# Performance work log

Hardware: AMD Instinct MI355X
Metric: run time of the kernel (lower is better)

Reference implementation:

```python
import jax, jax.numpy as jnp
import numpy as np

V, T, K, L, D = 256, 256, 36, 32, 1024
TAU = 0.05
MODE = 0
NEG_INF = -jnp.inf


def setup_inputs() -> dict:
    key = jax.random.key(0)
    k1, k2 = jax.random.split(key)
    imgs = jax.random.normal(k1, (V, K, D), dtype=jnp.float32)
    caps = jax.random.normal(k2, (T, L, D), dtype=jnp.float32)
    # Full lengths: the original module writes -inf into sim and 0 into w at
    # padded positions, so padding would produce -inf*0 = NaN in the output.
    img_lens = jnp.full((V,), K, dtype=jnp.int32)
    cap_lens = jnp.full((T,), L, dtype=jnp.int32)
    return {"imgs": imgs, "caps": caps, "img_lens": img_lens, "cap_lens": cap_lens}


def _l2norm(x):
    return x / jnp.maximum(jnp.linalg.norm(x, axis=-1, keepdims=True), 1e-12)


def reference(imgs, caps, img_lens, cap_lens):
    # masks: [V,K], [T,L]
    img_mask = (jnp.arange(K)[None, :] < img_lens[:, None]).astype(imgs.dtype)
    cap_mask = (jnp.arange(L)[None, :] < cap_lens[:, None]).astype(caps.dtype)
    # AvePool: masked mean over valid tokens, then L2-normalize
    img_glo = _l2norm((imgs * img_mask[:, :, None]).sum(1) / img_lens[:, None].astype(imgs.dtype))
    cap_glo = _l2norm((caps * cap_mask[:, :, None]).sum(1) / cap_lens[:, None].astype(caps.dtype))
    # ds: [V,T,K], et: [V,T,L]  (computed as in the original; note the original
    # forward overwrites w with the masked sim, so ds/et/softmax do not affect
    # the returned value — we keep only the live dataflow here)
    ds = jnp.einsum('vkd,td->vtk', imgs, cap_glo)
    et = jnp.einsum('tld,vd->vtl', caps, img_glo)
    del ds, et  # dead in the original (w is reassigned to masked sim)
    # sim: [V,T,K,L]
    sim = jnp.einsum('vkd,tld->vtkl', imgs, caps)
    sim_mask = img_mask[:, None, :, None] * cap_mask[None, :, None, :]  # [V,T,K,L]
    valid = sim_mask != 0
    sim = jnp.where(valid, sim, NEG_INF)
    # final w in the original is sim.masked_fill(sim_mask == 0, 0)
    w = jnp.where(valid, sim, 0.0)
    return jnp.einsum('vtkl,vtkl->vt', sim, w)
```

## Files before the change

kernel.cpp:

```cpp
#include <hip/hip_runtime.h>

#define V_N 256
#define T_N 256
#define K_N 36
#define L_N 32
#define D_N 1024
#define MROWS (V_N * K_N)
#define NROWS (T_N * L_N)
#define BM 128
#define BN 128
#define BK 64
#define KSTEPS (D_N / BK)
#define NBM (MROWS / BM)
#define NBN (NROWS / BN)
#define NWG (NBM * NBN)

typedef __attribute__((ext_vector_type(8))) short bf16x8;
typedef __attribute__((ext_vector_type(4))) float f32x4;
typedef __attribute__((ext_vector_type(16))) float f32x16;

#define SB0 __builtin_amdgcn_sched_barrier(0)
#define BAR __builtin_amdgcn_s_barrier()

__device__ __forceinline__ ushort f2bf(float x) {
  union { float f; unsigned int u; } c; c.f = x;
  unsigned int r = c.u + 0x7FFFu + ((c.u >> 16) & 1u);
  return (ushort)(r >> 16);
}

__global__ void cvt_a(const float* __restrict__ imgs, ushort* __restrict__ aws) {
  const int AQ = MROWS * (D_N / 4);
  for (int q = blockIdx.x * blockDim.x + threadIdx.x; q < AQ;
       q += gridDim.x * blockDim.x) {
    float4 f = reinterpret_cast<const float4*>(imgs)[q];
    ushort4 u; u.x = f2bf(f.x); u.y = f2bf(f.y); u.z = f2bf(f.z); u.w = f2bf(f.w);
    reinterpret_cast<ushort4*>(aws)[q] = u;
  }
}

__global__ void cvt_b2(const float* __restrict__ caps, ushort* __restrict__ b2) {
  const int NH = 256 * 64;
  int gid = blockIdx.x * blockDim.x + threadIdx.x;
  int h = gid >> 6;
  int lane = gid & 63;
  if (h >= NH) return;
  int c = h >> 6;
  int s = h & 63;
  int col = c * 32 + (lane & 31);
  int k   = s * 16 + ((lane >> 5) << 3);
  const float4* src = reinterpret_cast<const float4*>(caps + (size_t)col * D_N + k);
  float4 f0 = src[0], f1 = src[1];
  union { ushort u[8]; int4 v4; } pk;
  pk.u[0] = f2bf(f0.x); pk.u[1] = f2bf(f0.y); pk.u[2] = f2bf(f0.z); pk.u[3] = f2bf(f0.w);
  pk.u[4] = f2bf(f1.x); pk.u[5] = f2bf(f1.y); pk.u[6] = f2bf(f1.z); pk.u[7] = f2bf(f1.w);
  *reinterpret_cast<int4*>(b2 + (size_t)h * 512 + lane * 8) = pk.v4;
}

__global__ __launch_bounds__(256, 3) void gemm3(
    const ushort* __restrict__ aws, const ushort* __restrict__ b2,
    float* __restrict__ out) {
  __shared__ ushort lds[2 * BM * BK];

  int orig = (int)blockIdx.x;
  int xcd = orig & 7;
  int idx = orig >> 3;
  const int bn = xcd * 8 + (idx & 7);
  const int bm = idx >> 3;
  const int row0 = bm * BM;
  const int col0 = bn * BN;

  const int tid  = (int)threadIdx.x;
  const int lane = tid & 63;
  const int wid  = tid >> 6;
  const int wr   = wid >> 1;
  const int wc   = wid & 1;

  auto stageA = [&](int kt) {
    ushort* buf = lds + (kt & 1) * (BM * BK);
#pragma unroll
    for (int it = 0; it < 4; ++it) {
      int q = it * 256 + tid;
      int r = q >> 3;
      int sw = ((q & 7) << 4) ^ ((r & 7) << 4);
      const ushort* ga = aws + (size_t)(row0 + r) * D_N + kt * BK + (sw >> 1);
      __builtin_amdgcn_global_load_lds(
          (const __attribute__((address_space(1))) void*)ga,
          (__attribute__((address_space(3))) void*)(buf + q * 8), 16, 0, 0);
    }
  };

  auto rdA = [&](const ushort* buf, int mt, int ks) -> bf16x8 {
    int r = wr * 64 + mt * 32 + (lane & 31);
    int cb = ks * 32 + ((lane >> 5) << 4);
    int sw = cb ^ ((r & 7) << 4);
    return *reinterpret_cast<const bf16x8*>(buf + r * 64 + (sw >> 1));
  };

  const ushort* bbase = b2 + ((size_t)(bn * 4 + wc * 2) * 64) * 512 + lane * 8;
  auto ldB = [&](int t, int nt, int ks) -> bf16x8 {
    return *reinterpret_cast<const bf16x8*>(
        bbase + ((size_t)nt * 64 + t * 4 + ks) * 512);
  };

  f32x16 acc[2][2];
#pragma unroll
  for (int mt = 0; mt < 2; ++mt)
#pragma unroll
    for (int nt = 0; nt < 2; ++nt)
#pragma unroll
      for (int j = 0; j < 16; ++j) acc[mt][nt][j] = 0.f;

  stageA(0);
  asm volatile("s_waitcnt vmcnt(0)" ::: "memory");
  SB0; BAR; SB0;

  for (int t = 0; t < KSTEPS; ++t) {
    const ushort* buf = lds + (t & 1) * (BM * BK);
    if (t < KSTEPS - 1) stageA(t + 1);

    bf16x8 bB[8], aA[8];
#pragma unroll
    for (int ks = 0; ks < 4; ++ks) {
      bB[ks * 2]     = ldB(t, 0, ks);
      bB[ks * 2 + 1] = ldB(t, 1, ks);
    }
#pragma unroll
    for (int ks = 0; ks < 4; ++ks) {
      aA[ks * 2]     = rdA(buf, 0, ks);
      aA[ks * 2 + 1] = rdA(buf, 1, ks);
    }

#pragma unroll
    for (int ks = 0; ks < 4; ++ks)
#pragma unroll
      for (int mt = 0; mt < 2; ++mt)
#pragma unroll
        for (int nt = 0; nt < 2; ++nt)
          acc[mt][nt] = __builtin_amdgcn_mfma_f32_32x32x16_bf16(
              aA[ks * 2 + mt], bB[ks * 2 + nt], acc[mt][nt], 0, 0, 0);

    asm volatile("s_waitcnt vmcnt(0)" ::: "memory");
    SB0; BAR; SB0;
  }

#pragma unroll
  for (int mt = 0; mt < 2; ++mt) {
    int gbase = row0 + wr * 64 + mt * 32;
    int v0 = gbase / K_N;
    int b = (v0 + 1) * K_N;
#pragma unroll
    for (int nt = 0; nt < 2; ++nt) {
      f32x16 a = acc[mt][nt];
      float s0 = 0.f, s1 = 0.f;
#pragma unroll
      for (int j = 0; j < 16; ++j) {
        int row = (j & 3) + 8 * (j >> 2) + 4 * (lane >> 5);
        float x = a[j];
        float x2 = x * x;
        if (gbase + row < b) s0 += x2; else s1 += x2;
      }
#pragma unroll
      for (int off = 32; off > 0; off >>= 1) {
        s0 += __shfl_xor(s0, off, 64);
        s1 += __shfl_xor(s1, off, 64);
      }
      if (lane == 0) {
        int tcol = (col0 + wc * 64 + nt * 32) >> 5;
        atomicAdd(out + v0 * T_N + tcol, s0);
        if (b < gbase + 32) atomicAdd(out + (v0 + 1) * T_N + tcol, s1);
      }
    }
  }
}

__global__ __launch_bounds__(256) void gemm_fb(
    const float* __restrict__ imgs, const float* __restrict__ caps,
    float* __restrict__ out) {
  __shared__ ushort lds[128 * 64 + 128 * 64];
  ushort* ldsA = lds;
  ushort* ldsB = lds + 128 * 64;
  const int NBMf = MROWS / 128, NBNf = NROWS / 128;
  int orig = (int)blockIdx.x;
  int xcd = orig & 7;
  int idx = orig >> 3;
  int bn = xcd * (NBNf / 8) + (idx % (NBNf / 8));
  int bm = idx / (NBNf / 8);
  const int row0 = bm * 128, col0 = bn * 128;
  const int tid = (int)threadIdx.x, lane = tid & 63, wid = tid >> 6;
  const int wr = wid >> 1, wc = wid & 1;
  f32x4 acc[4][4];
#pragma unroll
  for (int i = 0; i < 4; ++i)
#pragma unroll
    for (int j = 0; j < 4; ++j) acc[i][j] = (f32x4){0.f, 0.f, 0.f, 0.f};
  for (int kt = 0; kt < KSTEPS; ++kt) {
#pragma unroll
    for (int it = 0; it < 4; ++it) {
      int q = it * 256 + tid;
      int r = q >> 3;
      int sw = ((q & 7) << 4) ^ ((r & 7) << 4);
      const float4* src = reinterpret_cast<const float4*>(
          imgs + (size_t)(row0 + r) * D_N + kt * BK + (sw >> 1));
      float4 f0 = src[0], f1 = src[1];
      union { ushort u[8]; int4 v4; } pk;
      pk.u[0] = f2bf(f0.x); pk.u[1] = f2bf(f0.y); pk.u[2] = f2bf(f0.z); pk.u[3] = f2bf(f0.w);
      pk.u[4] = f2bf(f1.x); pk.u[5] = f2bf(f1.y); pk.u[6] = f2bf(f1.z); pk.u[7] = f2bf(f1.w);
      *reinterpret_cast<int4*>(ldsA + q * 8) = pk.v4;
    }
#pragma unroll
    for (int it = 0; it < 4; ++it) {
      int q = it * 256 + tid;
      int r = q >> 3;
      int sw = ((q & 7) << 4) ^ ((r & 7) << 4);
      const float4* src = reinterpret_cast<const float4*>(
          caps + (size_t)(col0 + r) * D_N + kt * BK + (sw >> 1));
      float4 f0 = src[0], f1 = src[1];
      union { ushort u[8]; int4 v4; } pk;
      pk.u[0] = f2bf(f0.x); pk.u[1] = f2bf(f0.y); pk.u[2] = f2bf(f0.z); pk.u[3] = f2bf(f0.w);
      pk.u[4] = f2bf(f1.x); pk.u[5] = f2bf(f1.y); pk.u[6] = f2bf(f1.z); pk.u[7] = f2bf(f1.w);
      *reinterpret_cast<int4*>(ldsB + q * 8) = pk.v4;
    }
    __syncthreads();
#pragma unroll
    for (int ks = 0; ks < 2; ++ks) {
      bf16x8 afr[4], bfr[4];
#pragma unroll
      for (int i = 0; i < 4; ++i) {
        int r = wr * 64 + i * 16 + (lane & 15);
        int sw = (ks * 64 + (((lane >> 4) << 4))) ^ ((r & 7) << 4);
        afr[i] = *reinterpret_cast<const bf16x8*>(ldsA + r * BK + (sw >> 1));
      }
#pragma unroll
      for (int j = 0; j < 4; ++j) {
        int r = wc * 64 + j * 16 + (lane & 15);
        int sw = (ks * 64 + (((lane >> 4) << 4))) ^ ((r & 7) << 4);
        bfr[j] = *reinterpret_cast<const bf16x8*>(ldsB + r * BK + (sw >> 1));
      }
#pragma unroll
      for (int i = 0; i < 4; ++i)
#pragma unroll
        for (int j = 0; j < 4; ++j)
          acc[i][j] = __builtin_amdgcn_mfma_f32_16x16x32_bf16(afr[i], bfr[j], acc[i][j], 0, 0, 0);
    }
    __syncthreads();
  }
#pragma unroll
  for (int i = 0; i < 4; ++i) {
#pragma unroll
    for (int j = 0; j < 4; ++j) {
      f32x4 a4 = acc[i][j];
      int grow = row0 + wr * 64 + i * 16;
      int gcol = col0 + wc * 64 + j * 16;
      int t = gcol >> 5;
      int v0 = grow / K_N;
      int b = (v0 + 1) * K_N;
      int rbase = grow + ((lane >> 4) << 2);
      float s0 = 0.f, s1 = 0.f;
#pragma unroll
      for (int rg = 0; rg < 4; ++rg) {
        float x = a4[rg];
        float x2 = x * x;
        if (rbase + rg < b) s0 += x2; else s1 += x2;
      }
#pragma unroll
      for (int off = 32; off > 0; off >>= 1) {
        s0 += __shfl_xor(s0, off, 64);
        s1 += __shfl_xor(s1, off, 64);
      }
      if (lane == 0) {
        atomicAdd(out + v0 * T_N + t, s0);
        if (b < grow + 16) atomicAdd(out + (v0 + 1) * T_N + t, s1);
      }
    }
  }
}

extern "C" void kernel_launch(void* const* d_in, const int* in_sizes, int n_in,
                              void* d_out, int out_size, void* d_ws, size_t ws_size,
                              hipStream_t stream) {
  const float* imgs = (const float*)d_in[0];
  const float* caps = (const float*)d_in[1];
  float* out = (float*)d_out;

  hipMemsetAsync(d_out, 0, (size_t)V_N * T_N * sizeof(float), stream);

  const size_t need = (size_t)(MROWS + NROWS) * D_N * sizeof(ushort);

  if (ws_size >= need) {
    ushort* aws = (ushort*)d_ws;
    ushort* b2  = aws + (size_t)MROWS * D_N;
    cvt_a<<<2048, 256, 0, stream>>>(imgs, aws);
    cvt_b2<<<4096, 256, 0, stream>>>(caps, b2);
    gemm3<<<NWG, 256, 0, stream>>>(aws, b2, out);
  } else {
    const int nwg = (MROWS / 128) * (NROWS / 128);
    gemm_fb<<<nwg, 256, 0, stream>>>(imgs, caps, out);
  }
}
```

Baseline: 189.8 us.

## Drop LDS staging; load pre-swizzled MFMA fragments for A directly from global

Converts imgs into the same fragment-packed layout already used for caps, so each wave loads its A and B MFMA operands straight from global memory into registers with no LDS staging and no barriers. The M tile doubles to 256 rows, giving each wave a 4x2 grid of 32x32 accumulators, and loads are double-buffered in registers with explicit vmcnt waits to overlap loads and MFMAs. Occupancy drops to 2 workgroups per CU because of the higher register use. Operand reuse now relies on cache hits instead of shared memory, which may raise L2 traffic.

```diff
diff --git a/kernel.cpp b/kernel.cpp
--- a/kernel.cpp
+++ b/kernel.cpp
@@ -7,10 +7,9 @@
 #define D_N 1024
 #define MROWS (V_N * K_N)
 #define NROWS (T_N * L_N)
-#define BM 128
+#define BM 256
 #define BN 128
-#define BK 64
-#define KSTEPS (D_N / BK)
+#define KSTEPS 16
 #define NBM (MROWS / BM)
 #define NBN (NROWS / BN)
 #define NWG (NBM * NBN)
@@ -20,7 +19,6 @@
 typedef __attribute__((ext_vector_type(16))) float f32x16;
 
 #define SB0 __builtin_amdgcn_sched_barrier(0)
-#define BAR __builtin_amdgcn_s_barrier()
 
 __device__ __forceinline__ ushort f2bf(float x) {
   union { float f; unsigned int u; } c; c.f = x;
@@ -28,14 +26,22 @@
   return (ushort)(r >> 16);
 }
 
-__global__ void cvt_a(const float* __restrict__ imgs, ushort* __restrict__ aws) {
-  const int AQ = MROWS * (D_N / 4);
-  for (int q = blockIdx.x * blockDim.x + threadIdx.x; q < AQ;
-       q += gridDim.x * blockDim.x) {
-    float4 f = reinterpret_cast<const float4*>(imgs)[q];
-    ushort4 u; u.x = f2bf(f.x); u.y = f2bf(f.y); u.z = f2bf(f.z); u.w = f2bf(f.w);
-    reinterpret_cast<ushort4*>(aws)[q] = u;
-  }
+__global__ void cvt_a2(const float* __restrict__ imgs, ushort* __restrict__ a2) {
+  const int NH = (MROWS / 32) * 64;
+  int gid = blockIdx.x * blockDim.x + threadIdx.x;
+  int h = gid >> 6;
+  int lane = gid & 63;
+  if (h >= NH) return;
+  int rb = h >> 6;
+  int s  = h & 63;
+  int row = rb * 32 + (lane & 31);
+  int k   = s * 16 + ((lane >> 5) << 3);
+  const float4* src = reinterpret_cast<const float4*>(imgs + (size_t)row * D_N + k);
+  float4 f0 = src[0], f1 = src[1];
+  union { ushort u[8]; int4 v4; } pk;
+  pk.u[0] = f2bf(f0.x); pk.u[1] = f2bf(f0.y); pk.u[2] = f2bf(f0.z); pk.u[3] = f2bf(f0.w);
+  pk.u[4] = f2bf(f1.x); pk.u[5] = f2bf(f1.y); pk.u[6] = f2bf(f1.z); pk.u[7] = f2bf(f1.w);
+  *reinterpret_cast<int4*>(a2 + (size_t)h * 512 + lane * 8) = pk.v4;
 }
 
 __global__ void cvt_b2(const float* __restrict__ caps, ushort* __restrict__ b2) {
@@ -56,11 +62,9 @@
   *reinterpret_cast<int4*>(b2 + (size_t)h * 512 + lane * 8) = pk.v4;
 }
 
-__global__ __launch_bounds__(256, 3) void gemm3(
-    const ushort* __restrict__ aws, const ushort* __restrict__ b2,
+__global__ __launch_bounds__(256, 2) void gemm4(
+    const ushort* __restrict__ a2, const ushort* __restrict__ b2,
     float* __restrict__ out) {
-  __shared__ ushort lds[2 * BM * BK];
-
   int orig = (int)blockIdx.x;
   int xcd = orig & 7;
   int idx = orig >> 3;
@@ -75,77 +79,69 @@
   const int wr   = wid >> 1;
   const int wc   = wid & 1;
 
-  auto stageA = [&](int kt) {
-    ushort* buf = lds + (kt & 1) * (BM * BK);
-#pragma unroll
-    for (int it = 0; it < 4; ++it) {
-      int q = it * 256 + tid;
-      int r = q >> 3;
-      int sw = ((q & 7) << 4) ^ ((r & 7) << 4);
-      const ushort* ga = aws + (size_t)(row0 + r) * D_N + kt * BK + (sw >> 1);
-      __builtin_amdgcn_global_load_lds(
-          (const __attribute__((address_space(1))) void*)ga,
-          (__attribute__((address_space(3))) void*)(buf + q * 8), 16, 0, 0);
-    }
-  };
-
-  auto rdA = [&](const ushort* buf, int mt, int ks) -> bf16x8 {
-    int r = wr * 64 + mt * 32 + (lane & 31);
-    int cb = ks * 32 + ((lane >> 5) << 4);
-    int sw = cb ^ ((r & 7) << 4);
-    return *reinterpret_cast<const bf16x8*>(buf + r * 64 + (sw >> 1));
-  };
-
-  const ushort* bbase = b2 + ((size_t)(bn * 4 + wc * 2) * 64) * 512 + lane * 8;
-  auto ldB = [&](int t, int nt, int ks) -> bf16x8 {
-    return *reinterpret_cast<const bf16x8*>(
-        bbase + ((size_t)nt * 64 + t * 4 + ks) * 512);
-  };
-
-  f32x16 acc[2][2];
-#pragma unroll
-  for (int mt = 0; mt < 2; ++mt)
+  const ushort* aw = a2 + ((size_t)(bm * 8 + wr * 4) * 64) * 512 + lane * 8;
+  const ushort* bw = b2 + ((size_t)(bn * 4 + wc * 2) * 64) * 512 + lane * 8;
+
+
+  f32x16 acc[4][2];
+#pragma unroll
+  for (int mt = 0; mt < 4; ++mt)
 #pragma unroll
     for (int nt = 0; nt < 2; ++nt)
 #pragma unroll
       for (int j = 0; j < 16; ++j) acc[mt][nt][j] = 0.f;
 
-  stageA(0);
-  asm volatile("s_waitcnt vmcnt(0)" ::: "memory");
-  SB0; BAR; SB0;
+  bf16x8 A0[8], B0[4], A1[8], B1[4];
+
+#define ISSUE(Aset, Bset, t, p)                                              \
+  {                                                                          \
+    int s0 = (t) * 4 + (p) * 2;                                              \
+    _Pragma("unroll")                                                        \
+    for (int mt = 0; mt < 4; ++mt) {                                         \
+      Aset[mt * 2]     = *reinterpret_cast<const bf16x8*>(aw + ((size_t)mt * 64 + s0) * 512);     \
+      Aset[mt * 2 + 1] = *reinterpret_cast<const bf16x8*>(aw + ((size_t)mt * 64 + s0 + 1) * 512); \
+    }                                                                        \
+    _Pragma("unroll")                                                        \
+    for (int nt = 0; nt < 2; ++nt) {                                         \
+      Bset[nt * 2]     = *reinterpret_cast<const bf16x8*>(bw + ((size_t)nt * 64 + s0) * 512);     \
+      Bset[nt * 2 + 1] = *reinterpret_cast<const bf16x8*>(bw + ((size_t)nt * 64 + s0 + 1) * 512); \
+    }                                                                        \
+  }
+
+#define MFMA16(Aset, Bset)                                                   \
+  {                                                                          \
+    _Pragma("unroll")                                                        \
+    for (int ksl = 0; ksl < 2; ++ksl)                                        \
+      _Pragma("unroll")                                                      \
+      for (int mt = 0; mt < 4; ++mt)                                         \
+        _Pragma("unroll")                                                    \
+        for (int nt = 0; nt < 2; ++nt)                                       \
+          acc[mt][nt] = __builtin_amdgcn_mfma_f32_32x32x16_bf16(             \
+              Aset[mt * 2 + ksl], Bset[nt * 2 + ksl], acc[mt][nt], 0, 0, 0); \
+  }
+
+  ISSUE(A0, B0, 0, 0); SB0;
+  ISSUE(A1, B1, 0, 1); SB0;
 
   for (int t = 0; t < KSTEPS; ++t) {
-    const ushort* buf = lds + (t & 1) * (BM * BK);
-    if (t < KSTEPS - 1) stageA(t + 1);
-
-    bf16x8 bB[8], aA[8];
-#pragma unroll
-    for (int ks = 0; ks < 4; ++ks) {
-      bB[ks * 2]     = ldB(t, 0, ks);
-      bB[ks * 2 + 1] = ldB(t, 1, ks);
-    }
-#pragma unroll
-    for (int ks = 0; ks < 4; ++ks) {
-      aA[ks * 2]     = rdA(buf, 0, ks);
-      aA[ks * 2 + 1] = rdA(buf, 1, ks);
-    }
-
-#pragma unroll
-    for (int ks = 0; ks < 4; ++ks)
-#pragma unroll
-      for (int mt = 0; mt < 2; ++mt)
-#pragma unroll
-        for (int nt = 0; nt < 2; ++nt)
-          acc[mt][nt] = __builtin_amdgcn_mfma_f32_32x32x16_bf16(
-              aA[ks * 2 + mt], bB[ks * 2 + nt], acc[mt][nt], 0, 0, 0);
-
-    asm volatile("s_waitcnt vmcnt(0)" ::: "memory");
-    SB0; BAR; SB0;
-  }
-
-#pragma unroll
-  for (int mt = 0; mt < 2; ++mt) {
-    int gbase = row0 + wr * 64 + mt * 32;
+    asm volatile("s_waitcnt vmcnt(12)" ::: "memory");
+    SB0;
+    MFMA16(A0, B0);
+    SB0;
+    if (t < KSTEPS - 1) { ISSUE(A0, B0, t + 1, 0); }
+    SB0;
+    if (t < KSTEPS - 1) { asm volatile("s_waitcnt vmcnt(12)" ::: "memory"); }
+    else                { asm volatile("s_waitcnt vmcnt(0)"  ::: "memory"); }
+    SB0;
+    MFMA16(A1, B1);
+    SB0;
+    if (t < KSTEPS - 1) { ISSUE(A1, B1, t + 1, 1); }
+    SB0;
+  }
+
+#pragma unroll
+  for (int mt = 0; mt < 4; ++mt) {
+    int gbase = row0 + wr * 128 + mt * 32;
     int v0 = gbase / K_N;
     int b = (v0 + 1) * K_N;
 #pragma unroll
@@ -171,6 +167,8 @@
       }
     }
   }
+#undef ISSUE
+#undef MFMA16
 }
 
 __global__ __launch_bounds__(256) void gemm_fb(
@@ -200,7 +198,7 @@
       int r = q >> 3;
       int sw = ((q & 7) << 4) ^ ((r & 7) << 4);
       const float4* src = reinterpret_cast<const float4*>(
-          imgs + (size_t)(row0 + r) * D_N + kt * BK + (sw >> 1));
+          imgs + (size_t)(row0 + r) * D_N + kt * 64 + (sw >> 1));
       float4 f0 = src[0], f1 = src[1];
       union { ushort u[8]; int4 v4; } pk;
       pk.u[0] = f2bf(f0.x); pk.u[1] = f2bf(f0.y); pk.u[2] = f2bf(f0.z); pk.u[3] = f2bf(f0.w);
@@ -213,7 +211,7 @@
       int r = q >> 3;
       int sw = ((q & 7) << 4) ^ ((r & 7) << 4);
       const float4* src = reinterpret_cast<const float4*>(
-          caps + (size_t)(col0 + r) * D_N + kt * BK + (sw >> 1));
+          caps + (size_t)(col0 + r) * D_N + kt * 64 + (sw >> 1));
       float4 f0 = src[0], f1 = src[1];
       union { ushort u[8]; int4 v4; } pk;
       pk.u[0] = f2bf(f0.x); pk.u[1] = f2bf(f0.y); pk.u[2] = f2bf(f0.z); pk.u[3] = f2bf(f0.w);
@@ -228,13 +226,13 @@
       for (int i = 0; i < 4; ++i) {
         int r = wr * 64 + i * 16 + (lane & 15);
         int sw = (ks * 64 + (((lane >> 4) << 4))) ^ ((r & 7) << 4);
-        afr[i] = *reinterpret_cast<const bf16x8*>(ldsA + r * BK + (sw >> 1));
+        afr[i] = *reinterpret_cast<const bf16x8*>(ldsA + r * 64 + (sw >> 1));
       }
 #pragma unroll
       for (int j = 0; j < 4; ++j) {
         int r = wc * 64 + j * 16 + (lane & 15);
         int sw = (ks * 64 + (((lane >> 4) << 4))) ^ ((r & 7) << 4);
-        bfr[j] = *reinterpret_cast<const bf16x8*>(ldsB + r * BK + (sw >> 1));
+        bfr[j] = *reinterpret_cast<const bf16x8*>(ldsB + r * 64 + (sw >> 1));
       }
 #pragma unroll
       for (int i = 0; i < 4; ++i)
@@ -287,11 +285,11 @@
   const size_t need = (size_t)(MROWS + NROWS) * D_N * sizeof(ushort);
 
   if (ws_size >= need) {
-    ushort* aws = (ushort*)d_ws;
-    ushort* b2  = aws + (size_t)MROWS * D_N;
-    cvt_a<<<2048, 256, 0, stream>>>(imgs, aws);
+    ushort* a2 = (ushort*)d_ws;
+    ushort* b2 = a2 + (size_t)MROWS * D_N;
+    cvt_a2<<<4608, 256, 0, stream>>>(imgs, a2);
     cvt_b2<<<4096, 256, 0, stream>>>(caps, b2);
-    gemm3<<<NWG, 256, 0, stream>>>(aws, b2, out);
+    gemm4<<<NWG, 256, 0, stream>>>(a2, b2, out);
   } else {
     const int nwg = (MROWS / 128) * (NROWS / 128);
     gemm_fb<<<nwg, 256, 0, stream>>>(imgs, caps, out);
```

New measurement: 201.4 us. 6.1% more time.
